# Kernel optimization log

Hardware: AMD Instinct MI355X
Metric: run time of the kernel (lower is better)

Reference implementation:

```python
import jax, jax.numpy as jnp
import numpy as np

B, T, V, E, H, L = 64, 512, 256, 1024, 1024, 2


def setup_inputs() -> dict:
    key = jax.random.key(0)
    ks = jax.random.split(key, 9)
    s = 1.0 / np.sqrt(H)
    X = jax.random.randint(ks[0], (B, T), 0, V)
    h0 = jax.random.uniform(ks[1], (L, B, H), dtype=jnp.float32)
    emb = (jax.random.normal(ks[2], (V, E), dtype=jnp.float32) * 0.02).at[0].set(0.0)  # pad_idx=0 row zeroed
    W_ih = jax.random.normal(ks[3], (L, 3 * H, H), dtype=jnp.float32) * s
    W_hh = jax.random.normal(ks[4], (L, 3 * H, H), dtype=jnp.float32) * s
    b_ih = jax.random.normal(ks[5], (L, 3 * H), dtype=jnp.float32) * s
    b_hh = jax.random.normal(ks[6], (L, 3 * H), dtype=jnp.float32) * s
    W_out = jax.random.normal(ks[7], (V, H), dtype=jnp.float32) * s
    b_out = jax.random.normal(ks[8], (V,), dtype=jnp.float32) * s
    return {"X": X, "h0": h0, "emb": emb, "W_ih": W_ih, "W_hh": W_hh,
            "b_ih": b_ih, "b_hh": b_hh, "W_out": W_out, "b_out": b_out}


def _gru_layer(x, h0_l, W_ih_l, W_hh_l, b_ih_l, b_hh_l):
    # x: [B, T, D]; PyTorch GRU cell math (gate order r, z, n).
    gx = jnp.einsum('btd,gd->btg', x, W_ih_l) + b_ih_l  # [B, T, 3H], precomputed input GEMM

    def step(h, gx_t):  # gx_t: [B, 3H]
        gh = h @ W_hh_l.T + b_hh_l
        xr, xz, xn = jnp.split(gx_t, 3, axis=-1)
        hr, hz, hn = jnp.split(gh, 3, axis=-1)
        r = jax.nn.sigmoid(xr + hr)
        z = jax.nn.sigmoid(xz + hz)
        n = jnp.tanh(xn + r * hn)
        h_new = (1.0 - z) * n + z * h
        return h_new, h_new

    _, ys = jax.lax.scan(step, h0_l, jnp.swapaxes(gx, 0, 1))  # scan over time
    return jnp.swapaxes(ys, 0, 1)  # [B, T, H]


def reference(X, h0, emb, W_ih, W_hh, b_ih, b_hh, W_out, b_out):
    # Embedding lookup (dropout is identity in eval mode)
    x = emb[X]  # [B, T, E]
    for l in range(L):
        x = _gru_layer(x, h0[l], W_ih[l], W_hh[l], b_ih[l], b_hh[l])
    logits = jnp.einsum('bth,vh->btv', x, W_out) + b_out  # [B, T, V]
    # fptt returns out[:, :-1].reshape(-1, token_count)
    return logits[:, :-1, :].reshape(-1, V)
```

## Files before the change

kernel.cpp:

```cpp
#include <hip/hip_runtime.h>
#include <stdint.h>


namespace {

constexpr int B = 64, T = 512, V = 256, H = 1024, G = 3072;
constexpr int NBLK = 192;
constexpr int SLAB = 65536;
constexpr int R1MASK = 127;

typedef _Float16 f16;
typedef unsigned long long u64;
typedef f16 f16x8 __attribute__((ext_vector_type(8)));
typedef f16 f16x4 __attribute__((ext_vector_type(4)));
typedef float f32x4 __attribute__((ext_vector_type(4)));

#define MFMA16(av, bv, acc) __builtin_amdgcn_mfma_f32_16x16x32_f16(av, bv, acc, 0, 0, 0)

__device__ __forceinline__ f16x8 lload16(const f16* p) {
  return *reinterpret_cast<const f16x8*>(p);
}
__device__ __forceinline__ float lload2(const f16* p) { return (float)*p; }

__device__ __forceinline__ void astore2(f16* p, float v) {
  union { f16 f; unsigned short s; } u;
  u.f = (f16)v;
  __hip_atomic_store(reinterpret_cast<unsigned short*>(p), u.s,
                     __ATOMIC_RELAXED, __HIP_MEMORY_SCOPE_AGENT);
}
__device__ __forceinline__ float aloadf(const float* p) {
  return __hip_atomic_load(p, __ATOMIC_RELAXED, __HIP_MEMORY_SCOPE_AGENT);
}
__device__ __forceinline__ void astoref(float* p, float v) {
  __hip_atomic_store(p, v, __ATOMIC_RELAXED, __HIP_MEMORY_SCOPE_AGENT);
}
__device__ __forceinline__ void astorei(int* p, int v) {
  __hip_atomic_store(p, v, __ATOMIC_RELAXED, __HIP_MEMORY_SCOPE_AGENT);
}

__device__ __forceinline__ void poll3(const int* p0, const int* p1,
                                      const int* p2, int& a0, int& a1,
                                      int& a2) {
  asm volatile(
      "global_load_dword %0, %3, off sc1\n\t"
      "global_load_dword %1, %4, off sc1\n\t"
      "global_load_dword %2, %5, off sc1\n\t"
      "s_waitcnt vmcnt(0)"
      : "=&v"(a0), "=&v"(a1), "=&v"(a2)
      : "v"(p0), "v"(p1), "v"(p2)
      : "memory");
}

__device__ __forceinline__ void mm48(const f16* a, const f16* wp, f32x4& aR,
                                     f32x4& aZ, f32x4& aN) {
  f16x8 ring[8];
#pragma unroll
  for (int q = 0; q < 8; ++q) ring[q] = lload16(a + q * 2048);
#pragma unroll
  for (int k0 = 0; k0 < 32; ++k0) {
    f16x8 av = ring[k0 & 7];
    if (k0 + 8 < 32) ring[k0 & 7] = lload16(a + (k0 + 8) * 2048);
    const f16* w = wp + k0 * 1728;
    aR = MFMA16(av, *reinterpret_cast<const f16x8*>(w), aR);
    aZ = MFMA16(av, *reinterpret_cast<const f16x8*>(w + 576), aZ);
    aN = MFMA16(av, *reinterpret_cast<const f16x8*>(w + 1152), aN);
  }
}

__global__ void to_f16_4(const float* __restrict__ src, f16* __restrict__ dst,
                         int n4) {
  int i = blockIdx.x * 256 + threadIdx.x;
  if (i >= n4) return;
  float4 v = reinterpret_cast<const float4*>(src)[i];
  f16x4 o = {(f16)v.x, (f16)v.y, (f16)v.z, (f16)v.w};
  reinterpret_cast<f16x4*>(dst)[i] = o;
}

__global__ void pack_w(const float* __restrict__ Whh,
                       const float* __restrict__ Wih, f16* __restrict__ dst) {
  const int id = blockIdx.x * 256 + threadIdx.x;
  const int kkq = id & 3;
  const int rr = id >> 2;
  const int row = rr % 48;
  const int rest = rr / 48;
  const int k0 = rest & 31, bi = (rest >> 5) & 63, which = rest >> 11;
  const int g = row >> 4, jrow = row & 15;
  const float* base = (which == 0) ? Whh
                    : (which == 1) ? (Wih + (size_t)G * H)
                                   : (Whh + (size_t)G * H);
  const float* src =
      base + ((size_t)(g * H + bi * 16 + jrow)) * H + k0 * 32 + kkq * 8;
  float4 a = *reinterpret_cast<const float4*>(src);
  float4 b = *reinterpret_cast<const float4*>(src + 4);
  f16x8 o = {(f16)a.x, (f16)a.y, (f16)a.z, (f16)a.w,
             (f16)b.x, (f16)b.y, (f16)b.z, (f16)b.w};
  *reinterpret_cast<f16x8*>(dst + (size_t)id * 8) = o;
}

__global__ void pack_h0f(const float* __restrict__ h0, f16* __restrict__ h1r,
                         f16* __restrict__ h2r, int* __restrict__ bar) {
  if (blockIdx.x == 0 && threadIdx.x < NBLK) {
    bar[threadIdx.x * 16] = 0;
    bar[4096 + threadIdx.x * 16] = 0;
  }
  const int id = blockIdx.x * 256 + threadIdx.x;
  const int layer = id >> 16, b = (id >> 10) & 63, j = id & 1023;
  const size_t a = ((size_t)(j >> 5) * 64 + b) * 32 + (j & 31);
  const f16 v = (f16)h0[id];
  if (layer == 0) h1r[a] = v; else h2r[a] = v;
}

template <int MODE>
__global__ __launch_bounds__(256) void gemm_f16(
    const f16* __restrict__ A, const f16* __restrict__ Bm,
    const float* __restrict__ bias, float* __restrict__ C, int M, int N,
    int K) {
  __shared__ __align__(16) f16 As[64][48], Bs[64][48];

  const int tid = threadIdx.x;
  const int lane = tid & 63, wv = tid >> 6;
  const int bm = blockIdx.y, bn = blockIdx.x;
  const int srow = tid >> 2, sseg = (tid & 3) * 8;

  const f16* pA = (MODE == 2)
                      ? (A + (size_t)bm * 65536 + srow * 32 + sseg)
                      : (A + (size_t)(bm * 64 + srow) * K + sseg);
  const f16* pB = Bm + (size_t)(bn * 64 + srow) * K + sseg;

  f32x4 acc[4];
  const f32x4 zero = {0.f, 0.f, 0.f, 0.f};
#pragma unroll
  for (int nt = 0; nt < 4; ++nt) acc[nt] = zero;

  const int ar = wv * 16 + (lane & 15);
  const int kk = (lane >> 4) * 8;

  const int niter = K / 32;
  for (int ki = 0; ki < niter; ++ki) {
    int4 va = (MODE == 2) ? *reinterpret_cast<const int4*>(pA + ki * 2048)
                          : *reinterpret_cast<const int4*>(pA + ki * 32);
    int4 vb = *reinterpret_cast<const int4*>(pB + ki * 32);
    __syncthreads();
    *reinterpret_cast<int4*>(&As[srow][sseg]) = va;
    *reinterpret_cast<int4*>(&Bs[srow][sseg]) = vb;
    __syncthreads();

    f16x8 av = *reinterpret_cast<const f16x8*>(&As[ar][kk]);
#pragma unroll
    for (int nt = 0; nt < 4; ++nt) {
      f16x8 bv = *reinterpret_cast<const f16x8*>(&Bs[nt * 16 + (lane & 15)][kk]);
      acc[nt] = MFMA16(av, bv, acc[nt]);
    }
  }

  const int rbase = wv * 16 + (lane >> 4) * 4;
  const int cl = lane & 15;
#pragma unroll
  for (int nt = 0; nt < 4; ++nt) {
    const int n = bn * 64 + nt * 16 + cl;
    const float bv = bias[n];
#pragma unroll
    for (int r = 0; r < 4; ++r) {
      const int m = bm * 64 + rbase + r;
      const float v = acc[nt][r] + bv;
      if (MODE == 0) {
        C[(size_t)m * N + n] = v;
      } else {
        const int t = m >> 6, bb = m & 63;
        if (t < T - 1) C[((size_t)(bb * (T - 1) + t)) * V + n] = v;
      }
    }
  }
}

__global__ __launch_bounds__(256, 1) void gru_persist(
    const f16* __restrict__ pW, const float* __restrict__ G0,
    const int* __restrict__ X, const float* __restrict__ b_hh,
    const float* __restrict__ b_ih, f16* __restrict__ h1ring,
    f16* __restrict__ h2ring, float* __restrict__ gx2, int* __restrict__ bar) {
  __shared__ __align__(16) f16 Wt[55296];

  const int tid = threadIdx.x, bx = blockIdx.x;
  const int lane = tid & 63, wv = tid >> 6;
  const int l15 = lane & 15, kq = lane >> 4;
  const int role = bx >> 6, jb = bx & 63;

  int* arrive = bar;
  int* door = bar + 4096;

  {
    const int2* src = reinterpret_cast<const int2*>(pW + (size_t)bx * 49152);
#pragma unroll
    for (int q = 0; q < 48; ++q) {
      const int flat = q * 256 + tid;
      const int k0r = flat >> 3, seg = flat & 7;
      *reinterpret_cast<int2*>(&Wt[k0r * 36 + seg * 4]) = src[flat];
    }
  }
  __syncthreads();

  const int j = jb * 16 + l15;
  float br_ = 0.f, bz_ = 0.f, bn_ = 0.f, bxr_ = 0.f, bxz_ = 0.f, bxn_ = 0.f;
  if (role == 0) {
    br_ = b_hh[j]; bz_ = b_hh[H + j]; bn_ = b_hh[2 * H + j];
  } else if (role == 2) {
    br_ = b_hh[G + j]; bz_ = b_hh[G + H + j]; bn_ = b_hh[G + 2 * H + j];
    bxr_ = b_ih[G + j]; bxz_ = b_ih[G + H + j]; bxn_ = b_ih[G + 2 * H + j];
  }

  const int aoff = (wv * 16 + l15) * 32 + kq * 8;
  const f16* wp = Wt + l15 * 36 + kq * 8;
  const int bB = wv * 16 + kq * 4;
  const size_t hoff = (size_t)(j >> 5) * 2048 + (j & 31);

  for (int i = 0; i <= T + 1; ++i) {
    if (role == 0) {
      if (i < T) {
        const f16* hin = h1ring + (size_t)(i & R1MASK) * SLAB;
        f16* hout = h1ring + (size_t)((i + 1) & R1MASK) * SLAB;
        f32x4 aR = {0, 0, 0, 0}, aZ = {0, 0, 0, 0}, aN = {0, 0, 0, 0};
        mm48(hin + aoff, wp, aR, aZ, aN);
#pragma unroll
        for (int r = 0; r < 4; ++r) {
          const int b = bB + r;
          const float* gx = G0 + (size_t)X[b * T + i] * G;
          const float xr = gx[j], xz = gx[H + j], xn = gx[2 * H + j];
          const size_t ha = hoff + (size_t)b * 32;
          const float hp = lload2(hin + ha);
          const float rg = 1.f / (1.f + __expf(-(xr + aR[r] + br_)));
          const float zg = 1.f / (1.f + __expf(-(xz + aZ[r] + bz_)));
          const float ng = tanhf(xn + rg * (aN[r] + bn_));
          astore2(hout + ha, (1.f - zg) * ng + zg * hp);
        }
      }
    } else if (role == 1) {
      if (i >= 1 && i <= T) {
        const int t = i - 1;
        f32x4 aR = {0, 0, 0, 0}, aZ = {0, 0, 0, 0}, aN = {0, 0, 0, 0};
        mm48(h1ring + (size_t)(i & R1MASK) * SLAB + aoff, wp, aR, aZ, aN);
        float* gdst = gx2 + ((size_t)(t & 1) * 64 + jb) * 3072;
#pragma unroll
        for (int r = 0; r < 4; ++r) {
          const int b = bB + r;
          astoref(gdst + b * 16 + l15, aR[r]);
          astoref(gdst + 1024 + b * 16 + l15, aZ[r]);
          astoref(gdst + 2048 + b * 16 + l15, aN[r]);
        }
      }
    } else {
      if (i >= 2) {
        const int t = i - 2;
        const f16* hin = h2ring + (size_t)t * SLAB;
        f16* hout = h2ring + (size_t)(t + 1) * SLAB;
        const float* gsrc = gx2 + ((size_t)(t & 1) * 64 + jb) * 3072;
        f32x4 aR = {0, 0, 0, 0}, aZ = {0, 0, 0, 0}, aN = {0, 0, 0, 0};
        mm48(hin + aoff, wp, aR, aZ, aN);
#pragma unroll
        for (int r = 0; r < 4; ++r) {
          const int b = bB + r;
          const float xr = aloadf(gsrc + b * 16 + l15);
          const float xz = aloadf(gsrc + 1024 + b * 16 + l15);
          const float xn = aloadf(gsrc + 2048 + b * 16 + l15);
          const size_t ha = hoff + (size_t)b * 32;
          const float hp = lload2(hin + ha);
          const float rg = 1.f / (1.f + __expf(-(xr + bxr_ + aR[r] + br_)));
          const float zg = 1.f / (1.f + __expf(-(xz + bxz_ + aZ[r] + bz_)));
          const float ng = tanhf(xn + bxn_ + rg * (aN[r] + bn_));
          const float hv = (1.f - zg) * ng + zg * hp;
          astore2(hout + ha, hv);
        }
      }
    }

    asm volatile("s_waitcnt vmcnt(0)" ::: "memory");
    __builtin_amdgcn_sched_barrier(0);
    __syncthreads();
    const int ph = i + 1;
    if (tid == 0) astorei(&arrive[bx * 16], ph);
    if (bx == 0) {
      if (tid < 64) {
        int a0, a1, a2;
        for (;;) {
          poll3(&arrive[tid * 16], &arrive[(64 + tid) * 16],
                &arrive[(128 + tid) * 16], a0, a1, a2);
          if (__all(a0 >= ph && a1 >= ph && a2 >= ph)) break;
          __builtin_amdgcn_s_sleep(1);
        }
        astorei(&door[tid * 16], ph);
        astorei(&door[(64 + tid) * 16], ph);
        astorei(&door[(128 + tid) * 16], ph);
      }
    } else if (tid == 0) {
      while (__hip_atomic_load(&door[bx * 16], __ATOMIC_RELAXED,
                               __HIP_MEMORY_SCOPE_AGENT) < ph) {
        __builtin_amdgcn_s_sleep(1);
      }
    }
    __syncthreads();
    asm volatile("" ::: "memory");
  }
}

}

extern "C" void kernel_launch(void* const* d_in, const int* in_sizes, int n_in,
                              void* d_out, int out_size, void* d_ws,
                              size_t ws_size, hipStream_t stream) {
  const int* X = (const int*)d_in[0];
  const float* h0 = (const float*)d_in[1];
  const float* emb = (const float*)d_in[2];
  const float* W_ih = (const float*)d_in[3];
  const float* W_hh = (const float*)d_in[4];
  const float* b_ih = (const float*)d_in[5];
  const float* b_hh = (const float*)d_in[6];
  const float* W_out = (const float*)d_in[7];
  const float* b_out = (const float*)d_in[8];
  float* out = (float*)d_out;
  (void)in_sizes; (void)n_in; (void)out_size; (void)ws_size;

  char* p = (char*)d_ws;
  auto alloc = [&](size_t bytes) {
    char* q = p;
    p += (bytes + 255) & ~(size_t)255;
    return q;
  };
  f16* pW = (f16*)alloc((size_t)3 * 64 * 49152 * 2);
  float* G0 = (float*)alloc((size_t)V * G * 4);
  f16* emb16 = (f16*)alloc((size_t)V * H * 2);
  f16* wih0_16 = (f16*)alloc((size_t)G * H * 2);
  f16* wout16 = (f16*)alloc((size_t)V * H * 2);
  f16* h1ring = (f16*)alloc((size_t)128 * 65536 * 2);
  f16* h2ring = (f16*)alloc((size_t)513 * 65536 * 2);
  float* gx2 = (float*)alloc((size_t)2 * 64 * 3072 * 4);
  int* bar = (int*)alloc(32768);

  to_f16_4<<<(V * H / 4 + 255) / 256, 256, 0, stream>>>(emb, emb16, V * H / 4);
  to_f16_4<<<(G * H / 4 + 255) / 256, 256, 0, stream>>>(W_ih, wih0_16,
                                                        G * H / 4);
  to_f16_4<<<(V * H / 4 + 255) / 256, 256, 0, stream>>>(W_out, wout16,
                                                        V * H / 4);
  pack_w<<<4608, 256, 0, stream>>>(W_hh, W_ih, pW);
  pack_h0f<<<512, 256, 0, stream>>>(h0, h1ring, h2ring, bar);
  gemm_f16<0><<<dim3(G / 64, V / 64), 256, 0, stream>>>(emb16, wih0_16, b_ih,
                                                        G0, V, G, H);

  {
    const f16* a0 = pW; const float* a1 = G0; const int* a2 = X;
    const float* a3 = b_hh; const float* a4 = b_ih;
    f16* a5 = h1ring; f16* a6 = h2ring; float* a7 = gx2; int* a8 = bar;
    void* args[] = {&a0, &a1, &a2, &a3, &a4, &a5, &a6, &a7, &a8};
    hipLaunchCooperativeKernel((const void*)gru_persist, dim3(NBLK), dim3(256),
                               args, 0, stream);
  }

  gemm_f16<2><<<dim3(V / 64, T), 256, 0, stream>>>(h2ring + 65536, wout16,
                                                   b_out, out, T * B, V, H);
}
```

Measured before the change: 7.419 ms.

## Replace global lockstep barrier with per-role dataflow doors and extra sync blocks

Swaps the single all-block barrier, which each step had block 0 collect and then release, for three extra dedicated aggregator blocks. Each one tracks the minimum progress of one role group and publishes its own door counter. Worker blocks now wait only on the producer and consumer groups they depend on, so layer-1, the layer-2 input projection and layer-2 recurrence can drift apart within bounded slack. The gx2 staging buffer grows from 2 to 8 slots to allow that slack. This removes lockstep coupling and the barrier round-trip latency on the critical path, at the cost of more complex dependency reasoning and three extra spinning blocks.

```diff
diff --git a/kernel.cpp b/kernel.cpp
--- a/kernel.cpp
+++ b/kernel.cpp
@@ -5,7 +5,8 @@
 namespace {
 
 constexpr int B = 64, T = 512, V = 256, H = 1024, G = 3072;
-constexpr int NBLK = 192;
+constexpr int NWRK = 192;
+constexpr int NBLK = NWRK + 3;
 constexpr int SLAB = 65536;
 constexpr int R1MASK = 127;
 
@@ -37,18 +38,11 @@
 __device__ __forceinline__ void astorei(int* p, int v) {
   __hip_atomic_store(p, v, __ATOMIC_RELAXED, __HIP_MEMORY_SCOPE_AGENT);
 }
-
-__device__ __forceinline__ void poll3(const int* p0, const int* p1,
-                                      const int* p2, int& a0, int& a1,
-                                      int& a2) {
-  asm volatile(
-      "global_load_dword %0, %3, off sc1\n\t"
-      "global_load_dword %1, %4, off sc1\n\t"
-      "global_load_dword %2, %5, off sc1\n\t"
-      "s_waitcnt vmcnt(0)"
-      : "=&v"(a0), "=&v"(a1), "=&v"(a2)
-      : "v"(p0), "v"(p1), "v"(p2)
-      : "memory");
+__device__ __forceinline__ int aloadi(const int* p) {
+  return __hip_atomic_load(p, __ATOMIC_RELAXED, __HIP_MEMORY_SCOPE_AGENT);
+}
+__device__ __forceinline__ void waitge(const int* p, int target) {
+  while (aloadi(p) < target) __builtin_amdgcn_s_sleep(1);
 }
 
 __device__ __forceinline__ void mm48(const f16* a, const f16* wp, f32x4& aR,
@@ -99,9 +93,12 @@
 
 __global__ void pack_h0f(const float* __restrict__ h0, f16* __restrict__ h1r,
                          f16* __restrict__ h2r, int* __restrict__ bar) {
-  if (blockIdx.x == 0 && threadIdx.x < NBLK) {
-    bar[threadIdx.x * 16] = 0;
-    bar[4096 + threadIdx.x * 16] = 0;
+  if (blockIdx.x == 0 && threadIdx.x < NWRK) {
+    const int t4 = threadIdx.x * 16;
+    bar[t4] = 0;
+    bar[4096 + t4] = 0;
+    bar[8192 + t4] = 0;
+    bar[12288 + t4] = 0;
   }
   const int id = blockIdx.x * 256 + threadIdx.x;
   const int layer = id >> 16, b = (id >> 10) & 63, j = id & 1023;
@@ -181,12 +178,45 @@
   __shared__ __align__(16) f16 Wt[55296];
 
   const int tid = threadIdx.x, bx = blockIdx.x;
+
+  int* arrive = bar;
+
+  if (bx >= NWRK) {
+    const int r = bx - NWRK;
+    if (tid < 64) {
+      const int* slot = arrive + (r * 64 + tid) * 16;
+      int* dr = bar + 4096 * (1 + r);
+      const int lo = r + 1;
+      const int hi = (r == 0) ? 512 : 513;
+      int ph = lo;
+      while (ph <= hi) {
+        int m;
+        for (;;) {
+          m = aloadi(slot);
+#pragma unroll
+          for (int o = 32; o; o >>= 1) {
+            int t2 = __shfl_xor(m, o, 64);
+            m = m < t2 ? m : t2;
+          }
+          if (m >= ph) break;
+        }
+        if (m > hi) m = hi;
+        astorei(&dr[tid * 16], m);
+        astorei(&dr[(64 + tid) * 16], m);
+        astorei(&dr[(128 + tid) * 16], m);
+        ph = m + 1;
+      }
+    }
+    return;
+  }
+
   const int lane = tid & 63, wv = tid >> 6;
   const int l15 = lane & 15, kq = lane >> 4;
   const int role = bx >> 6, jb = bx & 63;
 
-  int* arrive = bar;
-  int* door = bar + 4096;
+  const int* door0 = bar + 4096 + bx * 16;
+  const int* door1 = bar + 8192 + bx * 16;
+  const int* door2 = bar + 12288 + bx * 16;
 
   {
     const int2* src = reinterpret_cast<const int2*>(pW + (size_t)bx * 49152);
@@ -213,91 +243,80 @@
   const int bB = wv * 16 + kq * 4;
   const size_t hoff = (size_t)(j >> 5) * 2048 + (j & 31);
 
-  for (int i = 0; i <= T + 1; ++i) {
+  const int i0 = (role == 0) ? 0 : (role == 1) ? 1 : 2;
+  const int i1 = (role == 0) ? (T - 1) : (role == 1) ? T : (T + 1);
+
+  for (int i = i0; i <= i1; ++i) {
+    if (tid == 0) {
+      if (role == 0) {
+        if (i >= 1) waitge(door0, i);
+        if (i >= 128) waitge(door1, i - 126);
+      } else if (role == 1) {
+        waitge(door0, i);
+        if (i >= 9) waitge(door2, i - 6);
+      } else {
+        waitge(door1, i);
+        if (i > 2) waitge(door2, i);
+      }
+    }
+    __syncthreads();
+
     if (role == 0) {
-      if (i < T) {
-        const f16* hin = h1ring + (size_t)(i & R1MASK) * SLAB;
-        f16* hout = h1ring + (size_t)((i + 1) & R1MASK) * SLAB;
-        f32x4 aR = {0, 0, 0, 0}, aZ = {0, 0, 0, 0}, aN = {0, 0, 0, 0};
-        mm48(hin + aoff, wp, aR, aZ, aN);
-#pragma unroll
-        for (int r = 0; r < 4; ++r) {
-          const int b = bB + r;
-          const float* gx = G0 + (size_t)X[b * T + i] * G;
-          const float xr = gx[j], xz = gx[H + j], xn = gx[2 * H + j];
-          const size_t ha = hoff + (size_t)b * 32;
-          const float hp = lload2(hin + ha);
-          const float rg = 1.f / (1.f + __expf(-(xr + aR[r] + br_)));
-          const float zg = 1.f / (1.f + __expf(-(xz + aZ[r] + bz_)));
-          const float ng = tanhf(xn + rg * (aN[r] + bn_));
-          astore2(hout + ha, (1.f - zg) * ng + zg * hp);
-        }
+      const f16* hin = h1ring + (size_t)(i & R1MASK) * SLAB;
+      f16* hout = h1ring + (size_t)((i + 1) & R1MASK) * SLAB;
+      f32x4 aR = {0, 0, 0, 0}, aZ = {0, 0, 0, 0}, aN = {0, 0, 0, 0};
+      mm48(hin + aoff, wp, aR, aZ, aN);
+#pragma unroll
+      for (int r = 0; r < 4; ++r) {
+        const int b = bB + r;
+        const float* gx = G0 + (size_t)X[b * T + i] * G;
+        const float xr = gx[j], xz = gx[H + j], xn = gx[2 * H + j];
+        const size_t ha = hoff + (size_t)b * 32;
+        const float hp = lload2(hin + ha);
+        const float rg = 1.f / (1.f + __expf(-(xr + aR[r] + br_)));
+        const float zg = 1.f / (1.f + __expf(-(xz + aZ[r] + bz_)));
+        const float ng = tanhf(xn + rg * (aN[r] + bn_));
+        astore2(hout + ha, (1.f - zg) * ng + zg * hp);
       }
     } else if (role == 1) {
-      if (i >= 1 && i <= T) {
-        const int t = i - 1;
-        f32x4 aR = {0, 0, 0, 0}, aZ = {0, 0, 0, 0}, aN = {0, 0, 0, 0};
-        mm48(h1ring + (size_t)(i & R1MASK) * SLAB + aoff, wp, aR, aZ, aN);
-        float* gdst = gx2 + ((size_t)(t & 1) * 64 + jb) * 3072;
-#pragma unroll
-        for (int r = 0; r < 4; ++r) {
-          const int b = bB + r;
-          astoref(gdst + b * 16 + l15, aR[r]);
-          astoref(gdst + 1024 + b * 16 + l15, aZ[r]);
-          astoref(gdst + 2048 + b * 16 + l15, aN[r]);
-        }
+      const int t = i - 1;
+      f32x4 aR = {0, 0, 0, 0}, aZ = {0, 0, 0, 0}, aN = {0, 0, 0, 0};
+      mm48(h1ring + (size_t)(i & R1MASK) * SLAB + aoff, wp, aR, aZ, aN);
+      float* gdst = gx2 + ((size_t)((t & 7) * 64 + jb)) * 3072;
+#pragma unroll
+      for (int r = 0; r < 4; ++r) {
+        const int b = bB + r;
+        astoref(gdst + b * 16 + l15, aR[r]);
+        astoref(gdst + 1024 + b * 16 + l15, aZ[r]);
+        astoref(gdst + 2048 + b * 16 + l15, aN[r]);
       }
     } else {
-      if (i >= 2) {
-        const int t = i - 2;
-        const f16* hin = h2ring + (size_t)t * SLAB;
-        f16* hout = h2ring + (size_t)(t + 1) * SLAB;
-        const float* gsrc = gx2 + ((size_t)(t & 1) * 64 + jb) * 3072;
-        f32x4 aR = {0, 0, 0, 0}, aZ = {0, 0, 0, 0}, aN = {0, 0, 0, 0};
-        mm48(hin + aoff, wp, aR, aZ, aN);
-#pragma unroll
-        for (int r = 0; r < 4; ++r) {
-          const int b = bB + r;
-          const float xr = aloadf(gsrc + b * 16 + l15);
-          const float xz = aloadf(gsrc + 1024 + b * 16 + l15);
-          const float xn = aloadf(gsrc + 2048 + b * 16 + l15);
-          const size_t ha = hoff + (size_t)b * 32;
-          const float hp = lload2(hin + ha);
-          const float rg = 1.f / (1.f + __expf(-(xr + bxr_ + aR[r] + br_)));
-          const float zg = 1.f / (1.f + __expf(-(xz + bxz_ + aZ[r] + bz_)));
-          const float ng = tanhf(xn + bxn_ + rg * (aN[r] + bn_));
-          const float hv = (1.f - zg) * ng + zg * hp;
-          astore2(hout + ha, hv);
-        }
+      const int t = i - 2;
+      const f16* hin = h2ring + (size_t)t * SLAB;
+      f16* hout = h2ring + (size_t)(t + 1) * SLAB;
+      const float* gsrc = gx2 + ((size_t)((t & 7) * 64 + jb)) * 3072;
+      f32x4 aR = {0, 0, 0, 0}, aZ = {0, 0, 0, 0}, aN = {0, 0, 0, 0};
+      mm48(hin + aoff, wp, aR, aZ, aN);
+#pragma unroll
+      for (int r = 0; r < 4; ++r) {
+        const int b = bB + r;
+        const float xr = aloadf(gsrc + b * 16 + l15);
+        const float xz = aloadf(gsrc + 1024 + b * 16 + l15);
+        const float xn = aloadf(gsrc + 2048 + b * 16 + l15);
+        const size_t ha = hoff + (size_t)b * 32;
+        const float hp = lload2(hin + ha);
+        const float rg = 1.f / (1.f + __expf(-(xr + bxr_ + aR[r] + br_)));
+        const float zg = 1.f / (1.f + __expf(-(xz + bxz_ + aZ[r] + bz_)));
+        const float ng = tanhf(xn + bxn_ + rg * (aN[r] + bn_));
+        const float hv = (1.f - zg) * ng + zg * hp;
+        astore2(hout + ha, hv);
       }
     }
 
     asm volatile("s_waitcnt vmcnt(0)" ::: "memory");
     __builtin_amdgcn_sched_barrier(0);
     __syncthreads();
-    const int ph = i + 1;
-    if (tid == 0) astorei(&arrive[bx * 16], ph);
-    if (bx == 0) {
-      if (tid < 64) {
-        int a0, a1, a2;
-        for (;;) {
-          poll3(&arrive[tid * 16], &arrive[(64 + tid) * 16],
-                &arrive[(128 + tid) * 16], a0, a1, a2);
-          if (__all(a0 >= ph && a1 >= ph && a2 >= ph)) break;
-          __builtin_amdgcn_s_sleep(1);
-        }
-        astorei(&door[tid * 16], ph);
-        astorei(&door[(64 + tid) * 16], ph);
-        astorei(&door[(128 + tid) * 16], ph);
-      }
-    } else if (tid == 0) {
-      while (__hip_atomic_load(&door[bx * 16], __ATOMIC_RELAXED,
-                               __HIP_MEMORY_SCOPE_AGENT) < ph) {
-        __builtin_amdgcn_s_sleep(1);
-      }
-    }
-    __syncthreads();
-    asm volatile("" ::: "memory");
+    if (tid == 0) astorei(&arrive[bx * 16], i + 1);
   }
 }
 
@@ -331,8 +350,8 @@
   f16* wout16 = (f16*)alloc((size_t)V * H * 2);
   f16* h1ring = (f16*)alloc((size_t)128 * 65536 * 2);
   f16* h2ring = (f16*)alloc((size_t)513 * 65536 * 2);
-  float* gx2 = (float*)alloc((size_t)2 * 64 * 3072 * 4);
-  int* bar = (int*)alloc(32768);
+  float* gx2 = (float*)alloc((size_t)8 * 64 * 3072 * 4);
+  int* bar = (int*)alloc(65536);
 
   to_f16_4<<<(V * H / 4 + 255) / 256, 256, 0, stream>>>(emb, emb16, V * H / 4);
   to_f16_4<<<(G * H / 4 + 255) / 256, 256, 0, stream>>>(W_ih, wih0_16,
```

Measured after the change: 7.654 ms. 3.2% more time.
